# Performance work log

Hardware: AMD Instinct MI355X
Metric: run time of the kernel (lower is better)

Reference implementation:

```python
import jax, jax.numpy as jnp
import numpy as np

N = 50000       # nodes
E = 800000      # edges (avg degree 16)
DIN = 128
DOUT = 128
ALPHA = 0.2     # leaky relu negative slope


def setup_inputs() -> dict:
    key = jax.random.key(0)
    k1, k2, k3, k4, k5 = jax.random.split(key, 5)
    h = jax.random.normal(k1, (N, DIN), dtype=jnp.float32)
    # xavier-normal-ish scaling for params
    W = jax.random.normal(k2, (DIN, DOUT), dtype=jnp.float32) * np.float32(np.sqrt(2.0 / (DIN + DOUT)))
    a = jax.random.normal(k3, (2 * DOUT,), dtype=jnp.float32) * np.float32(np.sqrt(2.0 / (2 * DOUT + 1)))
    src = jax.random.randint(k4, (E,), 0, N, dtype=jnp.int32)
    dst = jax.random.randint(k5, (E,), 0, N, dtype=jnp.int32)
    return {"h": h, "W": W, "a": a, "src": src, "dst": dst}


def reference(h, W, a, src, dst):
    # eval mode: dropout is a no-op (training=False)
    Wh = h @ W                                  # [N, DOUT]
    a_src, a_dst = a[:DOUT], a[DOUT:]
    s = Wh @ a_src                              # [N] per-node src score
    d = Wh @ a_dst                              # [N] per-node dst score
    e = jax.nn.leaky_relu(s[src] + d[dst], negative_slope=ALPHA)  # [E]
    # segment softmax over incoming edges of each dst node
    emax = jax.ops.segment_max(e, dst, num_segments=N)            # [N]
    emax = jnp.where(jnp.isfinite(emax), emax, jnp.float32(0.0))  # isolated nodes
    ex = jnp.exp(e - emax[dst])                                   # [E]
    denom = jax.ops.segment_sum(ex, dst, num_segments=N)          # [N]
    alpha = ex / denom[dst]                                       # [E]
    # weighted scatter-sum of src features into dst nodes
    h_out = jax.ops.segment_sum(alpha[:, None] * Wh[src], dst, num_segments=N)  # [N, DOUT]
    # residual: in_feats == out_feats -> Identity
    return h_out + h
```

## Files before the change

kernel.cpp:

```cpp
#include <hip/hip_runtime.h>
#include <math.h>

#define NN 50000
#define NE 800000
#define DD 128
#define LRELU 0.2f
#define CAP 64
#define SLICE 6256

typedef unsigned int uint;
typedef unsigned short ushort;
using short8 = __attribute__((ext_vector_type(8))) short;
using f32x4  = __attribute__((ext_vector_type(4))) float;

__device__ __forceinline__ uint pack_bf2(float x, float y) {
  uint a = __float_as_uint(x), b = __float_as_uint(y);
  a = (a + 0x7fffu + ((a >> 16) & 1u)) >> 16;
  b = (b + 0x7fffu + ((b >> 16) & 1u)) >> 16;
  return a | (b << 16);
}
__device__ __forceinline__ ushort pack_bf1(float x) {
  uint a = __float_as_uint(x);
  return (ushort)((a + 0x7fffu + ((a >> 16) & 1u)) >> 16);
}

__global__ __launch_bounds__(256) void k_prep(const float* __restrict__ W,
                                              const float* __restrict__ a,
                                              float* __restrict__ wsv,
                                              float* __restrict__ wdv,
                                              ushort* __restrict__ Wtg) {
  const int tid = threadIdx.x;
  if (tid < DD) {
    float accs = 0.f, accd = 0.f;
    for (int c = 0; c < DD; ++c) {
      float w = W[tid * DD + c];
      accs = fmaf(w, a[c], accs);
      accd = fmaf(w, a[DD + c], accd);
    }
    wsv[tid] = accs;
    wdv[tid] = accd;
  }
  for (int i = 0; i < 64; ++i) {
    int idx = tid * 64 + i;
    int c = idx >> 7, k = idx & 127;
    Wtg[idx] = pack_bf1(W[k * DD + c]);
  }
}

__global__ __launch_bounds__(256) void k_svdv(const float* __restrict__ h,
                                              const float* __restrict__ wsv,
                                              const float* __restrict__ wdv,
                                              float* __restrict__ sv,
                                              float* __restrict__ dv,
                                              ushort* __restrict__ h_b,
                                              int* __restrict__ cnt) {
  const int tid = threadIdx.x;
  if (tid < 16) cnt[blockIdx.x * 16 + tid] = 0;
  const int wave = tid >> 6, l = tid & 63;
  const int r = blockIdx.x * 16 + wave * 4 + (l >> 4);
  const int c8 = (l & 15) * 8;
  float4 h0 = *reinterpret_cast<const float4*>(h + (size_t)r * DD + c8);
  float4 h1 = *reinterpret_cast<const float4*>(h + (size_t)r * DD + c8 + 4);
  float4 w0 = *reinterpret_cast<const float4*>(wsv + c8);
  float4 w1 = *reinterpret_cast<const float4*>(wsv + c8 + 4);
  float4 d0 = *reinterpret_cast<const float4*>(wdv + c8);
  float4 d1 = *reinterpret_cast<const float4*>(wdv + c8 + 4);
  float ps = h0.x*w0.x + h0.y*w0.y + h0.z*w0.z + h0.w*w0.w
           + h1.x*w1.x + h1.y*w1.y + h1.z*w1.z + h1.w*w1.w;
  float pd = h0.x*d0.x + h0.y*d0.y + h0.z*d0.z + h0.w*d0.w
           + h1.x*d1.x + h1.y*d1.y + h1.z*d1.z + h1.w*d1.w;
#pragma unroll
  for (int off = 1; off < 16; off <<= 1) {
    ps += __shfl_xor(ps, off);
    pd += __shfl_xor(pd, off);
  }
  if ((l & 15) == 0) { sv[r] = ps; dv[r] = pd; }
  uint4 u;
  u.x = pack_bf2(h0.x, h0.y); u.y = pack_bf2(h0.z, h0.w);
  u.z = pack_bf2(h1.x, h1.y); u.w = pack_bf2(h1.z, h1.w);
  *reinterpret_cast<uint4*>(h_b + (size_t)r * DD + c8) = u;
}

__global__ __launch_bounds__(256) void k_mfma(const ushort* __restrict__ h_b,
                                              const ushort* __restrict__ Wtg,
                                              uint* __restrict__ Whb) {
  __shared__ ushort WtS[16384];
  __shared__ float stage[4][16][18];
  const int tid = threadIdx.x;

#pragma unroll
  for (int it = 0; it < 16; ++it) {
    int chunk = it * 256 + tid;
    int c = chunk >> 4, kc = chunk & 15;
    short8 v = *reinterpret_cast<const short8*>(Wtg + chunk * 8);
    *reinterpret_cast<short8*>(
        reinterpret_cast<char*>(WtS) + c * 256 + ((kc ^ (c & 7)) << 4)) = v;
  }
  __syncthreads();

  const int wave = tid >> 6, lane = tid & 63;
  const int rbase = blockIdx.x * 64 + wave * 16;
  const int arow = rbase + (lane & 15);
  const int asrc = arow < NN ? arow : 0;
  const bool rok = arow < NN;

  short8 afr[4];
#pragma unroll
  for (int kg = 0; kg < 4; ++kg)
    afr[kg] = *reinterpret_cast<const short8*>(
        h_b + (size_t)asrc * DD + kg * 32 + (lane >> 4) * 8);

  const int xb = lane & 7;
  for (int cb = 0; cb < 8; ++cb) {
    const int col = cb * 16 + (lane & 15);
    f32x4 acc = {0.f, 0.f, 0.f, 0.f};
#pragma unroll
    for (int kg = 0; kg < 4; ++kg) {
      int kchunk = kg * 4 + (lane >> 4);
      short8 bfr = *reinterpret_cast<const short8*>(
          reinterpret_cast<const char*>(WtS) + col * 256 + ((kchunk ^ xb) << 4));
      acc = __builtin_amdgcn_mfma_f32_16x16x32_bf16(afr[kg], bfr, acc, 0, 0, 0);
    }
    float (*st)[18] = stage[wave];
#pragma unroll
    for (int j = 0; j < 4; ++j) st[(lane >> 4) * 4 + j][lane & 15] = acc[j];
    __asm__ volatile("s_waitcnt lgkmcnt(0)" ::: "memory");
    __builtin_amdgcn_sched_barrier(0);
    if (rok) {
#pragma unroll
      for (int j2 = 0; j2 < 2; ++j2) {
        int p = (lane >> 4) + 4 * j2;
        float2 v = *reinterpret_cast<const float2*>(&st[lane & 15][2 * p]);
        Whb[(size_t)arow * 64 + cb * 8 + p] = pack_bf2(v.x, v.y);
      }
    }
    __asm__ volatile("s_waitcnt lgkmcnt(0)" ::: "memory");
    __builtin_amdgcn_sched_barrier(0);
  }
}

__global__ __launch_bounds__(256) void k_fill(const int* __restrict__ src,
                                              const int* __restrict__ dst,
                                              const float* __restrict__ sv,
                                              const float* __restrict__ dv,
                                              int* __restrict__ cnt,
                                              uint* __restrict__ entries) {
  const int xcd = blockIdx.x & 7;
  const int base = xcd * SLICE;
  const int e0 = (blockIdx.x >> 3) * 3125;
  const int e1 = e0 + 3125;
  const int t = threadIdx.x;

  for (int j0 = 0; j0 < 13; j0 += 4) {
    int idx[4], d[4];
    bool keep[4];
#pragma unroll
    for (int jj = 0; jj < 4; ++jj) {
      idx[jj] = e0 + (j0 + jj) * 256 + t;
      bool valid = idx[jj] < e1;
      d[jj] = valid ? dst[idx[jj]] : -1;
      keep[jj] = valid && ((uint)(d[jj] - base) < (uint)SLICE);
    }
    int s[4];
    float x[4];
#pragma unroll
    for (int jj = 0; jj < 4; ++jj)
      s[jj] = keep[jj] ? src[idx[jj]] : 0;
#pragma unroll
    for (int jj = 0; jj < 4; ++jj) {
      if (keep[jj]) {
        float ev = sv[s[jj]] + dv[d[jj]];
        ev = ev > 0.f ? ev : LRELU * ev;
        x[jj] = __expf(ev);
      }
    }
    int p[4];
#pragma unroll
    for (int jj = 0; jj < 4; ++jj)
      if (keep[jj]) p[jj] = atomicAdd(&cnt[d[jj]], 1);
#pragma unroll
    for (int jj = 0; jj < 4; ++jj)
      if (keep[jj] && p[jj] < CAP)
        entries[(size_t)d[jj] * CAP + p[jj]] =
            ((uint)pack_bf1(x[jj]) << 16) | (uint)s[jj];
  }
}

__global__ __launch_bounds__(256) void k_node(const float* __restrict__ h,
                                              const uint* __restrict__ Whb,
                                              const int* __restrict__ cnt,
                                              const uint* __restrict__ entries,
                                              float* __restrict__ out) {
  const int sl = blockIdx.x & 7;
  int wid = sl * SLICE + (blockIdx.x >> 3) * 4 + (threadIdx.x >> 6);
  const int lim = min(NN, (sl + 1) * SLICE);
  if (wid >= lim) return;
  wid = __builtin_amdgcn_readfirstlane(wid);
  const int lane = threadIdx.x & 63;

  float2 hrow = reinterpret_cast<const float2*>(h + (size_t)wid * DD)[lane];
  int deg = cnt[wid];
  deg = deg < CAP ? deg : CAP;
  float2* o2 = reinterpret_cast<float2*>(out + (size_t)wid * DD);
  if (deg == 0) { o2[lane] = hrow; return; }

  const uint* bucket = entries + (size_t)wid * CAP;
  const uint4* b4 = reinterpret_cast<const uint4*>(bucket);
  float2 ac0 = {0.f,0.f}, ac1 = {0.f,0.f}, ac2 = {0.f,0.f}, ac3 = {0.f,0.f};
  float den = 0.f;
  const int nq = deg >> 2;
  for (int q = 0; q < nq; ++q) {
    uint4 e4 = b4[q];
    float x0 = __uint_as_float(e4.x & 0xffff0000u);
    float x1 = __uint_as_float(e4.y & 0xffff0000u);
    float x2 = __uint_as_float(e4.z & 0xffff0000u);
    float x3 = __uint_as_float(e4.w & 0xffff0000u);
    uint u0 = Whb[(size_t)(e4.x & 0xffffu) * 64 + lane];
    uint u1 = Whb[(size_t)(e4.y & 0xffffu) * 64 + lane];
    uint u2 = Whb[(size_t)(e4.z & 0xffffu) * 64 + lane];
    uint u3 = Whb[(size_t)(e4.w & 0xffffu) * 64 + lane];
    den += (x0 + x1) + (x2 + x3);
    ac0.x = fmaf(x0, __uint_as_float(u0 << 16), ac0.x);
    ac0.y = fmaf(x0, __uint_as_float(u0 & 0xffff0000u), ac0.y);
    ac1.x = fmaf(x1, __uint_as_float(u1 << 16), ac1.x);
    ac1.y = fmaf(x1, __uint_as_float(u1 & 0xffff0000u), ac1.y);
    ac2.x = fmaf(x2, __uint_as_float(u2 << 16), ac2.x);
    ac2.y = fmaf(x2, __uint_as_float(u2 & 0xffff0000u), ac2.y);
    ac3.x = fmaf(x3, __uint_as_float(u3 << 16), ac3.x);
    ac3.y = fmaf(x3, __uint_as_float(u3 & 0xffff0000u), ac3.y);
  }
  for (int k = nq * 4; k < deg; ++k) {
    uint e = bucket[k];
    float x0 = __uint_as_float(e & 0xffff0000u);
    uint u0 = Whb[(size_t)(e & 0xffffu) * 64 + lane];
    den += x0;
    ac0.x = fmaf(x0, __uint_as_float(u0 << 16), ac0.x);
    ac0.y = fmaf(x0, __uint_as_float(u0 & 0xffff0000u), ac0.y);
  }
  float inv = 1.0f / den;
  float ax = (ac0.x + ac1.x) + (ac2.x + ac3.x);
  float ay = (ac0.y + ac1.y) + (ac2.y + ac3.y);
  o2[lane] = make_float2(hrow.x + ax * inv, hrow.y + ay * inv);
}

extern "C" void kernel_launch(void* const* d_in, const int* in_sizes, int n_in,
                              void* d_out, int out_size, void* d_ws, size_t ws_size,
                              hipStream_t stream) {
  const float* h = (const float*)d_in[0];
  const float* W = (const float*)d_in[1];
  const float* a = (const float*)d_in[2];
  const int* src = (const int*)d_in[3];
  const int* dst = (const int*)d_in[4];
  float* out = (float*)d_out;

  char* ws = (char*)d_ws;
  uint*   Whb     = (uint*)  (ws);
  ushort* h_b     = (ushort*)(ws + 12800000);
  uint*   entries = (uint*)  (ws + 25600000);
  ushort* Wtg     = (ushort*)(ws + 38400000);
  float*  sv      = (float*) (ws + 38432768);
  float*  dv      = (float*) (ws + 38632768);
  float*  wsv     = (float*) (ws + 38832768);
  float*  wdv     = (float*) (ws + 38833280);
  int*    cnt     = (int*)   (ws + 38833792);

  hipLaunchKernelGGL(k_prep, dim3(1), dim3(256), 0, stream, W, a, wsv, wdv, Wtg);
  hipLaunchKernelGGL(k_svdv, dim3(3125), dim3(256), 0, stream,
                     h, wsv, wdv, sv, dv, h_b, cnt);
  hipLaunchKernelGGL(k_fill, dim3(2048), dim3(256), 0, stream,
                     src, dst, sv, dv, cnt, entries);
  hipLaunchKernelGGL(k_mfma, dim3(782), dim3(256), 0, stream, h_b, Wtg, Whb);
  hipLaunchKernelGGL(k_node, dim3(8 * (SLICE / 4)), dim3(256), 0, stream,
                     h, Whb, cnt, entries, out);
}
```

Before: 185.8 us.

## Fuse score computation and bf16 conversion into the MFMA GEMM kernel

Merges the per-node score/bf16-conversion kernel into the MFMA projection kernel, so h is converted to bf16 straight into swizzled shared memory instead of being written to and reread from a global h_b buffer. This also drops one launch. The weight-transpose prep now runs across 64 blocks instead of one thread block looping. The edge fill loop is simplified to a plain strided loop with atomicExch stores, giving up the 4-way batched load ILP and possibly adding atomic store cost.

```diff
diff --git a/kernel.cpp b/kernel.cpp
--- a/kernel.cpp
+++ b/kernel.cpp
@@ -30,63 +30,39 @@
                                               float* __restrict__ wdv,
                                               ushort* __restrict__ Wtg) {
   const int tid = threadIdx.x;
-  if (tid < DD) {
+  int idx = blockIdx.x * 256 + tid;
+  int c = idx >> 7, k = idx & 127;
+  Wtg[idx] = pack_bf1(W[k * DD + c]);
+
+  if (blockIdx.x == 0 && tid < DD) {
     float accs = 0.f, accd = 0.f;
-    for (int c = 0; c < DD; ++c) {
-      float w = W[tid * DD + c];
-      accs = fmaf(w, a[c], accs);
-      accd = fmaf(w, a[DD + c], accd);
+    for (int cc = 0; cc < DD; ++cc) {
+      float w = W[tid * DD + cc];
+      accs = fmaf(w, a[cc], accs);
+      accd = fmaf(w, a[DD + cc], accd);
     }
     wsv[tid] = accs;
     wdv[tid] = accd;
   }
-  for (int i = 0; i < 64; ++i) {
-    int idx = tid * 64 + i;
-    int c = idx >> 7, k = idx & 127;
-    Wtg[idx] = pack_bf1(W[k * DD + c]);
-  }
-}
-
-__global__ __launch_bounds__(256) void k_svdv(const float* __restrict__ h,
-                                              const float* __restrict__ wsv,
-                                              const float* __restrict__ wdv,
-                                              float* __restrict__ sv,
-                                              float* __restrict__ dv,
-                                              ushort* __restrict__ h_b,
-                                              int* __restrict__ cnt) {
-  const int tid = threadIdx.x;
-  if (tid < 16) cnt[blockIdx.x * 16 + tid] = 0;
-  const int wave = tid >> 6, l = tid & 63;
-  const int r = blockIdx.x * 16 + wave * 4 + (l >> 4);
-  const int c8 = (l & 15) * 8;
-  float4 h0 = *reinterpret_cast<const float4*>(h + (size_t)r * DD + c8);
-  float4 h1 = *reinterpret_cast<const float4*>(h + (size_t)r * DD + c8 + 4);
-  float4 w0 = *reinterpret_cast<const float4*>(wsv + c8);
-  float4 w1 = *reinterpret_cast<const float4*>(wsv + c8 + 4);
-  float4 d0 = *reinterpret_cast<const float4*>(wdv + c8);
-  float4 d1 = *reinterpret_cast<const float4*>(wdv + c8 + 4);
-  float ps = h0.x*w0.x + h0.y*w0.y + h0.z*w0.z + h0.w*w0.w
-           + h1.x*w1.x + h1.y*w1.y + h1.z*w1.z + h1.w*w1.w;
-  float pd = h0.x*d0.x + h0.y*d0.y + h0.z*d0.z + h0.w*d0.w
-           + h1.x*d1.x + h1.y*d1.y + h1.z*d1.z + h1.w*d1.w;
-#pragma unroll
-  for (int off = 1; off < 16; off <<= 1) {
-    ps += __shfl_xor(ps, off);
-    pd += __shfl_xor(pd, off);
-  }
-  if ((l & 15) == 0) { sv[r] = ps; dv[r] = pd; }
-  uint4 u;
-  u.x = pack_bf2(h0.x, h0.y); u.y = pack_bf2(h0.z, h0.w);
-  u.z = pack_bf2(h1.x, h1.y); u.w = pack_bf2(h1.z, h1.w);
-  *reinterpret_cast<uint4*>(h_b + (size_t)r * DD + c8) = u;
-}
-
-__global__ __launch_bounds__(256) void k_mfma(const ushort* __restrict__ h_b,
-                                              const ushort* __restrict__ Wtg,
-                                              uint* __restrict__ Whb) {
+}
+
+__global__ __launch_bounds__(256) void k_gemm2(const float* __restrict__ h,
+                                               const float* __restrict__ wsv,
+                                               const float* __restrict__ wdv,
+                                               const ushort* __restrict__ Wtg,
+                                               float* __restrict__ sv,
+                                               float* __restrict__ dv,
+                                               uint* __restrict__ Whb,
+                                               int* __restrict__ cnt) {
   __shared__ ushort WtS[16384];
+  __shared__ ushort hbs[8192];
   __shared__ float stage[4][16][18];
   const int tid = threadIdx.x;
+
+  if (tid < 64) {
+    int idx = blockIdx.x * 64 + tid;
+    if (idx < NN) cnt[idx] = 0;
+  }
 
 #pragma unroll
   for (int it = 0; it < 16; ++it) {
@@ -96,19 +72,52 @@
     *reinterpret_cast<short8*>(
         reinterpret_cast<char*>(WtS) + c * 256 + ((kc ^ (c & 7)) << 4)) = v;
   }
+
+  const int wave = tid >> 6, l = tid & 63;
+  const int cg = l & 15;
+  const int c8 = cg * 8;
+  float4 w0 = *reinterpret_cast<const float4*>(wsv + c8);
+  float4 w1 = *reinterpret_cast<const float4*>(wsv + c8 + 4);
+  float4 d0 = *reinterpret_cast<const float4*>(wdv + c8);
+  float4 d1 = *reinterpret_cast<const float4*>(wdv + c8 + 4);
+#pragma unroll
+  for (int rr = 0; rr < 4; ++rr) {
+    int row = wave * 16 + rr * 4 + (l >> 4);
+    int grow = blockIdx.x * 64 + row;
+    int gsrc = grow < NN ? grow : 0;
+    float4 h0 = *reinterpret_cast<const float4*>(h + (size_t)gsrc * DD + c8);
+    float4 h1 = *reinterpret_cast<const float4*>(h + (size_t)gsrc * DD + c8 + 4);
+    float ps = h0.x*w0.x + h0.y*w0.y + h0.z*w0.z + h0.w*w0.w
+             + h1.x*w1.x + h1.y*w1.y + h1.z*w1.z + h1.w*w1.w;
+    float pd = h0.x*d0.x + h0.y*d0.y + h0.z*d0.z + h0.w*d0.w
+             + h1.x*d1.x + h1.y*d1.y + h1.z*d1.z + h1.w*d1.w;
+#pragma unroll
+    for (int off = 1; off < 16; off <<= 1) {
+      ps += __shfl_xor(ps, off);
+      pd += __shfl_xor(pd, off);
+    }
+    if (cg == 0 && grow < NN) { sv[grow] = ps; dv[grow] = pd; }
+    uint4 u;
+    u.x = pack_bf2(h0.x, h0.y); u.y = pack_bf2(h0.z, h0.w);
+    u.z = pack_bf2(h1.x, h1.y); u.w = pack_bf2(h1.z, h1.w);
+    *reinterpret_cast<uint4*>(
+        reinterpret_cast<char*>(hbs) + row * 256 + ((cg ^ (row & 7)) << 4)) = u;
+  }
   __syncthreads();
 
-  const int wave = tid >> 6, lane = tid & 63;
-  const int rbase = blockIdx.x * 64 + wave * 16;
-  const int arow = rbase + (lane & 15);
-  const int asrc = arow < NN ? arow : 0;
-  const bool rok = arow < NN;
+  const int lane = l;
+  const int arow16 = lane & 15;
+  const int garow = blockIdx.x * 64 + wave * 16 + arow16;
+  const bool rok = garow < NN;
 
   short8 afr[4];
 #pragma unroll
-  for (int kg = 0; kg < 4; ++kg)
+  for (int kg = 0; kg < 4; ++kg) {
+    int row = wave * 16 + arow16;
+    int g = kg * 4 + (lane >> 4);
     afr[kg] = *reinterpret_cast<const short8*>(
-        h_b + (size_t)asrc * DD + kg * 32 + (lane >> 4) * 8);
+        reinterpret_cast<const char*>(hbs) + row * 256 + ((g ^ (row & 7)) << 4));
+  }
 
   const int xb = lane & 7;
   for (int cb = 0; cb < 8; ++cb) {
@@ -131,7 +140,7 @@
       for (int j2 = 0; j2 < 2; ++j2) {
         int p = (lane >> 4) + 4 * j2;
         float2 v = *reinterpret_cast<const float2*>(&st[lane & 15][2 * p]);
-        Whb[(size_t)arow * 64 + cb * 8 + p] = pack_bf2(v.x, v.y);
+        Whb[(size_t)garow * 64 + cb * 8 + p] = pack_bf2(v.x, v.y);
       }
     }
     __asm__ volatile("s_waitcnt lgkmcnt(0)" ::: "memory");
@@ -149,40 +158,17 @@
   const int base = xcd * SLICE;
   const int e0 = (blockIdx.x >> 3) * 3125;
   const int e1 = e0 + 3125;
-  const int t = threadIdx.x;
-
-  for (int j0 = 0; j0 < 13; j0 += 4) {
-    int idx[4], d[4];
-    bool keep[4];
-#pragma unroll
-    for (int jj = 0; jj < 4; ++jj) {
-      idx[jj] = e0 + (j0 + jj) * 256 + t;
-      bool valid = idx[jj] < e1;
-      d[jj] = valid ? dst[idx[jj]] : -1;
-      keep[jj] = valid && ((uint)(d[jj] - base) < (uint)SLICE);
-    }
-    int s[4];
-    float x[4];
-#pragma unroll
-    for (int jj = 0; jj < 4; ++jj)
-      s[jj] = keep[jj] ? src[idx[jj]] : 0;
-#pragma unroll
-    for (int jj = 0; jj < 4; ++jj) {
-      if (keep[jj]) {
-        float ev = sv[s[jj]] + dv[d[jj]];
-        ev = ev > 0.f ? ev : LRELU * ev;
-        x[jj] = __expf(ev);
-      }
-    }
-    int p[4];
-#pragma unroll
-    for (int jj = 0; jj < 4; ++jj)
-      if (keep[jj]) p[jj] = atomicAdd(&cnt[d[jj]], 1);
-#pragma unroll
-    for (int jj = 0; jj < 4; ++jj)
-      if (keep[jj] && p[jj] < CAP)
-        entries[(size_t)d[jj] * CAP + p[jj]] =
-            ((uint)pack_bf1(x[jj]) << 16) | (uint)s[jj];
+  for (int i = e0 + threadIdx.x; i < e1; i += 256) {
+    int d = dst[i];
+    if ((uint)(d - base) >= (uint)SLICE) continue;
+    int s = src[i];
+    float ev = sv[s] + dv[d];
+    ev = ev > 0.f ? ev : LRELU * ev;
+    float x = __expf(ev);
+    int p = atomicAdd(&cnt[d], 1);
+    if (p < CAP)
+      atomicExch(&entries[(size_t)d * CAP + p],
+                 ((uint)pack_bf1(x) << 16) | (uint)s);
   }
 }
 
@@ -255,21 +241,19 @@
 
   char* ws = (char*)d_ws;
   uint*   Whb     = (uint*)  (ws);
-  ushort* h_b     = (ushort*)(ws + 12800000);
-  uint*   entries = (uint*)  (ws + 25600000);
-  ushort* Wtg     = (ushort*)(ws + 38400000);
-  float*  sv      = (float*) (ws + 38432768);
-  float*  dv      = (float*) (ws + 38632768);
-  float*  wsv     = (float*) (ws + 38832768);
-  float*  wdv     = (float*) (ws + 38833280);
-  int*    cnt     = (int*)   (ws + 38833792);
-
-  hipLaunchKernelGGL(k_prep, dim3(1), dim3(256), 0, stream, W, a, wsv, wdv, Wtg);
-  hipLaunchKernelGGL(k_svdv, dim3(3125), dim3(256), 0, stream,
-                     h, wsv, wdv, sv, dv, h_b, cnt);
+  uint*   entries = (uint*)  (ws + 12800000);
+  ushort* Wtg     = (ushort*)(ws + 25600000);
+  float*  sv      = (float*) (ws + 25632768);
+  float*  dv      = (float*) (ws + 25832768);
+  float*  wsv     = (float*) (ws + 26032768);
+  float*  wdv     = (float*) (ws + 26033280);
+  int*    cnt     = (int*)   (ws + 26033792);
+
+  hipLaunchKernelGGL(k_prep, dim3(64), dim3(256), 0, stream, W, a, wsv, wdv, Wtg);
+  hipLaunchKernelGGL(k_gemm2, dim3(782), dim3(256), 0, stream,
+                     h, wsv, wdv, Wtg, sv, dv, Whb, cnt);
   hipLaunchKernelGGL(k_fill, dim3(2048), dim3(256), 0, stream,
                      src, dst, sv, dv, cnt, entries);
-  hipLaunchKernelGGL(k_mfma, dim3(782), dim3(256), 0, stream, h_b, Wtg, Whb);
   hipLaunchKernelGGL(k_node, dim3(8 * (SLICE / 4)), dim3(256), 0, stream,
                      h, Whb, cnt, entries, out);
 }
```

After: 198.5 us. 6.8% more time.
